# Kernel tuning notes

Hardware: AMD Instinct MI355X
Metric: run time of the kernel (lower is better)

The kernel has to match this reference:

```python
import jax, jax.numpy as jnp
import numpy as np

N_NODES = 50000  # nodes in the (sub)graph


def setup_inputs() -> dict:
    key = jax.random.key(0)
    ks = jax.random.split(key, 8)
    nodes = jax.random.randint(ks[0], (N_NODES,), 0, 100000)
    src = jax.random.randint(ks[1], (800000,), 0, N_NODES)
    dst = jax.random.randint(ks[2], (800000,), 0, N_NODES)
    emb = jax.random.normal(ks[3], (100000, 256), dtype=jnp.float32)
    W = jax.random.normal(ks[4], (256, 128), dtype=jnp.float32) * 0.05
    b = jax.random.normal(ks[5], (128,), dtype=jnp.float32) * 0.05
    mlp_w = jax.random.normal(ks[6], (128, 40), dtype=jnp.float32) * 0.05
    mlp_b = jax.random.normal(ks[7], (40,), dtype=jnp.float32) * 0.05
    return {"nodes": nodes, "src": src, "dst": dst, "emb": emb,
            "W": W, "b": b, "mlp_w": mlp_w, "mlp_b": mlp_b}


def reference(nodes, src, dst, emb, W, b, mlp_w, mlp_b):
    n = N_NODES
    ones = jnp.ones_like(src, dtype=jnp.float32)
    out_deg = jax.ops.segment_sum(ones, src, num_segments=n)  # src out-degree
    in_deg = jax.ops.segment_sum(ones, dst, num_segments=n)   # dst in-degree
    norm_src = jax.lax.rsqrt(jnp.maximum(out_deg, 1.0))       # D_out^{-1/2}
    norm_dst = jax.lax.rsqrt(jnp.maximum(in_deg, 1.0))        # D_in^{-1/2}

    feat = emb[nodes]                                          # [N, in_dim]
    # dgl GraphConv(norm='both'): in_dim > out_dim -> project first, then aggregate
    h = (feat * norm_src[:, None]) @ W                         # [N, out_dim]
    agg = jax.ops.segment_sum(h[src], dst, num_segments=n)     # SpMM: sum over in-edges
    feat_out = agg * norm_dst[:, None] + b                     # [N, out_dim]

    logits = feat_out @ mlp_w + mlp_b                          # [N, num_classes]
    return (feat_out, logits)
```

## Files before the change

kernel.cpp:

```cpp
#include <hip/hip_runtime.h>

#define IN_DIM 256
#define OUT_DIM 128
#define N_CLS 40

#define SLICE 8192
#define NE_CH 20

typedef __attribute__((ext_vector_type(8))) short short8;
typedef __attribute__((ext_vector_type(4))) float floatx4;

static __device__ __forceinline__ unsigned short f2bf(float f) {
    union { float f; unsigned u; } v; v.f = f;
    unsigned r = v.u + 0x7FFF + ((v.u >> 16) & 1);
    return (unsigned short)(r >> 16);
}

__global__ __launch_bounds__(256) void hist_wconv_kernel(
    const int* __restrict__ src, const int* __restrict__ dst,
    int* __restrict__ partial_out, int* __restrict__ partial_in,
    const float* __restrict__ W, unsigned short* __restrict__ Wt,
    int ne, int n, int chunk, int nbh)
{
    __shared__ __align__(16) int lh_out[SLICE];
    __shared__ __align__(16) int lh_in[SLICE];

    const int tid = threadIdx.x;

    if (blockIdx.x >= nbh) {
        int t = (blockIdx.x - nbh) * 256 + tid;
        if (t < IN_DIM * OUT_DIM) {
            int k = t >> 7, c = t & 127;
            Wt[c * IN_DIM + k] = f2bf(W[t]);
        }
        return;
    }

    const int s = blockIdx.x / NE_CH;
    const int e = blockIdx.x % NE_CH;
    const int lo = s * SLICE;
    const int hi = min(lo + SLICE, n);

    for (int i = tid; i < SLICE; i += 256) { lh_out[i] = 0; lh_in[i] = 0; }
    __syncthreads();

    const int start = e * chunk;
    const int end = min(start + chunk, ne);
    const int cnt4 = (end - start) >> 2;
    const int4* s4 = (const int4*)(src + start);
    const int4* d4 = (const int4*)(dst + start);
    for (int k = tid; k < cnt4; k += 256) {
        int4 sv = s4[k];
        int4 dv = d4[k];
        unsigned q;
        q = (unsigned)(sv.x - lo); if (q < SLICE) atomicAdd(&lh_out[q], 1);
        q = (unsigned)(sv.y - lo); if (q < SLICE) atomicAdd(&lh_out[q], 1);
        q = (unsigned)(sv.z - lo); if (q < SLICE) atomicAdd(&lh_out[q], 1);
        q = (unsigned)(sv.w - lo); if (q < SLICE) atomicAdd(&lh_out[q], 1);
        q = (unsigned)(dv.x - lo); if (q < SLICE) atomicAdd(&lh_in[q], 1);
        q = (unsigned)(dv.y - lo); if (q < SLICE) atomicAdd(&lh_in[q], 1);
        q = (unsigned)(dv.z - lo); if (q < SLICE) atomicAdd(&lh_in[q], 1);
        q = (unsigned)(dv.w - lo); if (q < SLICE) atomicAdd(&lh_in[q], 1);
    }
    for (int t = start + (cnt4 << 2) + tid; t < end; t += 256) {
        unsigned q;
        q = (unsigned)(src[t] - lo); if (q < SLICE) atomicAdd(&lh_out[q], 1);
        q = (unsigned)(dst[t] - lo); if (q < SLICE) atomicAdd(&lh_in[q], 1);
    }
    __syncthreads();

    const int cnt = hi - lo;
    const int c4 = cnt >> 2;
    int4* po = (int4*)(partial_out + (size_t)e * n + lo);
    int4* pi = (int4*)(partial_in + (size_t)e * n + lo);
    for (int i = tid; i < c4; i += 256) {
        po[i] = ((const int4*)lh_out)[i];
        pi[i] = ((const int4*)lh_in)[i];
    }
    for (int i = (c4 << 2) + tid; i < cnt; i += 256) {
        partial_out[(size_t)e * n + lo + i] = lh_out[i];
        partial_in[(size_t)e * n + lo + i] = lh_in[i];
    }
}

__global__ __launch_bounds__(256) void reduce_kernel(
    int* __restrict__ partial_out, int* __restrict__ partial_in,
    int* __restrict__ cnt_out, int* __restrict__ cnt_in, int n)
{
    const int g = blockIdx.x * 256 + threadIdx.x;
    const int ng4 = n >> 2;
    if (g < ng4) {
        const size_t base = (size_t)g * 4;
        int4 sum = make_int4(0, 0, 0, 0);
#pragma unroll
        for (int e = 0; e < NE_CH; e++) {
            int4 v = *(const int4*)(partial_out + (size_t)e * n + base);
            sum.x += v.x; sum.y += v.y; sum.z += v.z; sum.w += v.w;
        }
        *(int4*)(cnt_out + base) = sum;

        int4 run = make_int4(0, 0, 0, 0);
#pragma unroll
        for (int e = 0; e < NE_CH; e++) {
            int* p = partial_in + (size_t)e * n + base;
            int4 v = *(const int4*)p;
            *(int4*)p = run;
            run.x += v.x; run.y += v.y; run.z += v.z; run.w += v.w;
        }
        *(int4*)(cnt_in + base) = run;
    }
    const int t = (ng4 << 2) + g;
    if (t < n) {
        int sum = 0;
#pragma unroll
        for (int e = 0; e < NE_CH; e++) sum += partial_out[(size_t)e * n + t];
        cnt_out[t] = sum;
        int run = 0;
#pragma unroll
        for (int e = 0; e < NE_CH; e++) {
            int v = partial_in[(size_t)e * n + t];
            partial_in[(size_t)e * n + t] = run;
            run += v;
        }
        cnt_in[t] = run;
    }
}

__global__ __launch_bounds__(1024) void scan_kernel(
    const int* __restrict__ cnt, int* __restrict__ row_start, int n)
{
    __shared__ int wsum[16];
    __shared__ int carry_s;
    const int tid = threadIdx.x;
    const int lane = tid & 63, wid = tid >> 6;
    if (tid == 0) carry_s = 0;
    __syncthreads();

    for (int chunk = 0; chunk < n; chunk += 8192) {
        int base = chunk + tid * 8;
        int v[8];
        if (base + 8 <= n) {
            int4 a = *(const int4*)&cnt[base];
            int4 b = *(const int4*)&cnt[base + 4];
            v[0]=a.x; v[1]=a.y; v[2]=a.z; v[3]=a.w;
            v[4]=b.x; v[5]=b.y; v[6]=b.z; v[7]=b.w;
        } else {
#pragma unroll
            for (int t = 0; t < 8; t++) v[t] = (base + t < n) ? cnt[base + t] : 0;
        }
        int tsum = 0;
#pragma unroll
        for (int t = 0; t < 8; t++) tsum += v[t];

        int incl = tsum;
#pragma unroll
        for (int off = 1; off < 64; off <<= 1) {
            int q = __shfl_up(incl, (unsigned)off, 64);
            if (lane >= off) incl += q;
        }
        if (lane == 63) wsum[wid] = incl;
        __syncthreads();
        int woff = 0;
        for (int w = 0; w < wid; ++w) woff += wsum[w];
        int carry = carry_s;
        int run = carry + woff + (incl - tsum);
        if (base + 8 <= n) {
            int o[8];
#pragma unroll
            for (int t = 0; t < 8; t++) { o[t] = run; run += v[t]; }
            int4 r0, r1;
            r0.x=o[0]; r0.y=o[1]; r0.z=o[2]; r0.w=o[3];
            r1.x=o[4]; r1.y=o[5]; r1.z=o[6]; r1.w=o[7];
            *(int4*)&row_start[base]     = r0;
            *(int4*)&row_start[base + 4] = r1;
        } else {
#pragma unroll
            for (int t = 0; t < 8; t++) {
                if (base + t < n) row_start[base + t] = run;
                run += v[t];
            }
        }
        __syncthreads();
        if (tid == 1023) carry_s = carry + woff + incl;
        __syncthreads();
    }
    if (tid == 0) row_start[n] = carry_s;
}

__global__ __launch_bounds__(256) void scatter_lds_kernel(
    const int* __restrict__ src, const int* __restrict__ dst,
    const int* __restrict__ row_start, const int* __restrict__ prefix_in,
    int* __restrict__ csr_src, int ne, int n, int chunk)
{
    __shared__ __align__(16) int cur[SLICE];

    const int tid = threadIdx.x;
    const int s = blockIdx.x / NE_CH;
    const int e = blockIdx.x % NE_CH;
    const int lo = s * SLICE;
    const int hi = min(lo + SLICE, n);
    const int cnt = hi - lo;

    const int c4 = cnt >> 2;
    for (int i = tid; i < c4; i += 256) {
        int4 rs = *(const int4*)(row_start + lo + i * 4);
        int4 pf = *(const int4*)(prefix_in + (size_t)e * n + lo + i * 4);
        rs.x += pf.x; rs.y += pf.y; rs.z += pf.z; rs.w += pf.w;
        ((int4*)cur)[i] = rs;
    }
    for (int i = (c4 << 2) + tid; i < cnt; i += 256)
        cur[i] = row_start[lo + i] + prefix_in[(size_t)e * n + lo + i];
    __syncthreads();

    const int start = e * chunk;
    const int end = min(start + chunk, ne);
    const int cnt4e = (end - start) >> 2;
    const int4* s4 = (const int4*)(src + start);
    const int4* d4 = (const int4*)(dst + start);
    for (int k = tid; k < cnt4e; k += 256) {
        int4 sv = s4[k];
        int4 dv = d4[k];
        unsigned q;
        q = (unsigned)(dv.x - lo); if (q < SLICE) csr_src[atomicAdd(&cur[q], 1)] = sv.x;
        q = (unsigned)(dv.y - lo); if (q < SLICE) csr_src[atomicAdd(&cur[q], 1)] = sv.y;
        q = (unsigned)(dv.z - lo); if (q < SLICE) csr_src[atomicAdd(&cur[q], 1)] = sv.z;
        q = (unsigned)(dv.w - lo); if (q < SLICE) csr_src[atomicAdd(&cur[q], 1)] = sv.w;
    }
    for (int t = start + (cnt4e << 2) + tid; t < end; t += 256) {
        unsigned q = (unsigned)(dst[t] - lo);
        if (q < SLICE) csr_src[atomicAdd(&cur[q], 1)] = src[t];
    }
}

__global__ __launch_bounds__(256) void gemm1_mfma_kernel(
    const int* __restrict__ nodes, const float* __restrict__ emb,
    const unsigned short* __restrict__ Wt, const int* __restrict__ cnt_out,
    unsigned short* __restrict__ h, int n)
{
    __shared__ unsigned short A_lds[128 * 40];
    __shared__ unsigned short B_lds[128 * 40];
    __shared__ int   snode[128];
    __shared__ float sscale[128];

    const int tid = threadIdx.x;
    const int m0  = blockIdx.x * 128;

    if (tid < 128) {
        int gr = m0 + tid;
        snode[tid]  = (gr < n) ? nodes[gr] : 0;
        sscale[tid] = (gr < n) ? rsqrtf(fmaxf((float)cnt_out[gr], 1.0f)) : 0.0f;
    }
    __syncthreads();

    const int arow = tid >> 1, aq = tid & 1;
    const float* aptr = emb + (size_t)snode[arow] * IN_DIM + aq * 16;
    const unsigned short* bptr = Wt + arow * IN_DIM + aq * 16;

    float    ar[16];
    unsigned bw[8];

#define LOAD_REGS(KK) do {                                           \
        _Pragma("unroll")                                            \
        for (int q = 0; q < 4; q++) {                                \
            const floatx4 v = *(const floatx4*)(aptr + (KK) * 32 + q * 4); \
            ar[q*4+0]=v[0]; ar[q*4+1]=v[1]; ar[q*4+2]=v[2]; ar[q*4+3]=v[3]; \
        }                                                            \
        const uint4 w0 = *(const uint4*)(bptr + (KK) * 32);          \
        const uint4 w1 = *(const uint4*)(bptr + (KK) * 32 + 8);      \
        bw[0]=w0.x; bw[1]=w0.y; bw[2]=w0.z; bw[3]=w0.w;              \
        bw[4]=w1.x; bw[5]=w1.y; bw[6]=w1.z; bw[7]=w1.w;              \
    } while (0)

#define WRITE_LDS() do {                                             \
        union { unsigned short s[16]; uint4 v[2]; } ua;              \
        _Pragma("unroll")                                            \
        for (int i = 0; i < 16; i++) ua.s[i] = f2bf(ar[i]);          \
        *(uint4*)&A_lds[arow * 40 + aq * 16]     = ua.v[0];          \
        *(uint4*)&A_lds[arow * 40 + aq * 16 + 8] = ua.v[1];          \
        uint4 b0, b1;                                                \
        b0.x=bw[0]; b0.y=bw[1]; b0.z=bw[2]; b0.w=bw[3];              \
        b1.x=bw[4]; b1.y=bw[5]; b1.z=bw[6]; b1.w=bw[7];              \
        *(uint4*)&B_lds[arow * 40 + aq * 16]     = b0;               \
        *(uint4*)&B_lds[arow * 40 + aq * 16 + 8] = b1;               \
    } while (0)

    const int wave = tid >> 6, lane = tid & 63;
    const int wr = (wave & 1) * 64;
    const int wc = (wave >> 1) * 64;
    const int fr = lane & 15;
    const int koff = (lane >> 4) * 8;

    floatx4 acc[4][4];
#pragma unroll
    for (int i = 0; i < 4; i++)
#pragma unroll
        for (int j = 0; j < 4; j++) acc[i][j] = (floatx4){0.f, 0.f, 0.f, 0.f};

    LOAD_REGS(0);
    WRITE_LDS();

    for (int kk = 0; kk < 8; ++kk) {
        if (kk < 7) LOAD_REGS(kk + 1);
        __syncthreads();
        short8 af[4], bf[4];
#pragma unroll
        for (int t = 0; t < 4; t++) {
            af[t] = *(const short8*)&A_lds[(wr + t * 16 + fr) * 40 + koff];
            bf[t] = *(const short8*)&B_lds[(wc + t * 16 + fr) * 40 + koff];
        }
#pragma unroll
        for (int rt = 0; rt < 4; rt++)
#pragma unroll
            for (int ct = 0; ct < 4; ct++)
                acc[rt][ct] = __builtin_amdgcn_mfma_f32_16x16x32_bf16(
                    bf[ct], af[rt], acc[rt][ct], 0, 0, 0);
        __syncthreads();
        if (kk < 7) WRITE_LDS();
    }

#pragma unroll
    for (int rt = 0; rt < 4; rt++) {
        int lrow = wr + rt * 16 + fr;
        int grow = m0 + lrow;
        float sc = sscale[lrow];
        if (grow < n) {
#pragma unroll
            for (int ct = 0; ct < 4; ct++) {
                int col = wc + ct * 16 + (lane >> 4) * 4;
                union { unsigned short s[4]; uint2 v; } o;
                o.s[0] = f2bf(acc[rt][ct][0] * sc);
                o.s[1] = f2bf(acc[rt][ct][1] * sc);
                o.s[2] = f2bf(acc[rt][ct][2] * sc);
                o.s[3] = f2bf(acc[rt][ct][3] * sc);
                *(uint2*)&h[(size_t)grow * OUT_DIM + col] = o.v;
            }
        }
    }
#undef LOAD_REGS
#undef WRITE_LDS
}

__global__ __launch_bounds__(256) void spmm_csr_kernel(
    const int* __restrict__ row_start, const int* __restrict__ csr_src,
    const unsigned short* __restrict__ h, const float* __restrict__ bias,
    float* __restrict__ out_feat, int n)
{
    const int lane = threadIdx.x & 63;
    const int c2 = lane * 2;
    const int row = blockIdx.x * 4 + (threadIdx.x >> 6);
    if (row >= n) return;

    const int rs = row_start[row];
    const int re = row_start[row + 1];
    const int deg = re - rs;

    float aL[4] = {0.f, 0.f, 0.f, 0.f};
    float aH[4] = {0.f, 0.f, 0.f, 0.f};

    for (int base = 0; base < deg; base += 64) {
        const int cnt = min(deg - base, 64);
        int idx = (lane < cnt) ? csr_src[rs + base + lane] : 0;
        int t = 0;
        for (; t + 15 < cnt; t += 16) {
            int s[16];
#pragma unroll
            for (int u = 0; u < 16; u++) s[u] = __shfl(idx, t + u, 64);
            unsigned v[16];
#pragma unroll
            for (int u = 0; u < 16; u++)
                v[u] = *(const unsigned*)&h[(size_t)s[u] * OUT_DIM + c2];
#pragma unroll
            for (int u = 0; u < 16; u++) {
                union { unsigned uu; float f; } x, y;
                x.uu = v[u] << 16;
                y.uu = v[u] & 0xffff0000u;
                aL[u & 3] += x.f;
                aH[u & 3] += y.f;
            }
        }
        for (; t + 3 < cnt; t += 4) {
            int s[4];
#pragma unroll
            for (int u = 0; u < 4; u++) s[u] = __shfl(idx, t + u, 64);
            unsigned v[4];
#pragma unroll
            for (int u = 0; u < 4; u++)
                v[u] = *(const unsigned*)&h[(size_t)s[u] * OUT_DIM + c2];
#pragma unroll
            for (int u = 0; u < 4; u++) {
                union { unsigned uu; float f; } x, y;
                x.uu = v[u] << 16;
                y.uu = v[u] & 0xffff0000u;
                aL[u] += x.f;
                aH[u] += y.f;
            }
        }
        for (; t < cnt; ++t) {
            int s0 = __shfl(idx, t, 64);
            unsigned v0 = *(const unsigned*)&h[(size_t)s0 * OUT_DIM + c2];
            union { unsigned uu; float f; } x, y;
            x.uu = v0 << 16;
            y.uu = v0 & 0xffff0000u;
            aL[0] += x.f;
            aH[0] += y.f;
        }
    }

    const float nd = rsqrtf(fmaxf((float)deg, 1.0f));
    const float f0 = ((aL[0] + aL[1]) + (aL[2] + aL[3])) * nd + bias[c2];
    const float f1 = ((aH[0] + aH[1]) + (aH[2] + aH[3])) * nd + bias[c2 + 1];
    union { float f[2]; unsigned long long u; } o;
    o.f[0] = f0; o.f[1] = f1;
    __builtin_nontemporal_store(o.u,
        (unsigned long long*)&out_feat[(size_t)row * OUT_DIM + c2]);
}

__global__ __launch_bounds__(256) void mlp_mfma_kernel(
    const float* __restrict__ F, const float* __restrict__ mlp_w,
    const float* __restrict__ mlp_b, float* __restrict__ out_logits, int n)
{
    __shared__ unsigned short A_lds[48 * 136];
    __shared__ float s_mlpb[48];

    const int tid = threadIdx.x;
    for (int i = tid; i < 48 * 128; i += 256) {
        int cls = i >> 7, k = i & 127;
        A_lds[cls * 136 + k] =
            (cls < N_CLS) ? f2bf(mlp_w[(size_t)k * N_CLS + cls]) : (unsigned short)0;
    }
    if (tid < 48) s_mlpb[tid] = (tid < N_CLS) ? mlp_b[tid] : 0.f;
    __syncthreads();

    const int wave = tid >> 6, lane = tid & 63;
    const int r = lane & 15, koff = (lane >> 4) * 8;
    const int row = blockIdx.x * 64 + wave * 16 + r;
    const int rowc = (row < n) ? row : (n - 1);
    const float* fp = F + (size_t)rowc * OUT_DIM + koff;

    floatx4 acc[3];
#pragma unroll
    for (int ct = 0; ct < 3; ct++) acc[ct] = (floatx4){0.f, 0.f, 0.f, 0.f};

#pragma unroll
    for (int kk = 0; kk < 4; kk++) {
        floatx4 v0 = *(const floatx4*)(fp + kk * 32);
        floatx4 v1 = *(const floatx4*)(fp + kk * 32 + 4);
        union { unsigned short s[8]; short8 v; } bfr;
#pragma unroll
        for (int i = 0; i < 4; i++) {
            bfr.s[i]     = f2bf(v0[i]);
            bfr.s[4 + i] = f2bf(v1[i]);
        }
#pragma unroll
        for (int ct = 0; ct < 3; ct++) {
            short8 af = *(const short8*)&A_lds[(ct * 16 + r) * 136 + kk * 32 + koff];
            acc[ct] = __builtin_amdgcn_mfma_f32_16x16x32_bf16(af, bfr.v, acc[ct], 0, 0, 0);
        }
    }

    if (row < n) {
#pragma unroll
        for (int ct = 0; ct < 3; ct++)
#pragma unroll
            for (int i = 0; i < 4; i++) {
                int cls = ct * 16 + (lane >> 4) * 4 + i;
                if (cls < N_CLS)
                    __builtin_nontemporal_store(acc[ct][i] + s_mlpb[cls],
                        &out_logits[(size_t)row * N_CLS + cls]);
            }
    }
}

extern "C" void kernel_launch(void* const* d_in, const int* in_sizes, int n_in,
                              void* d_out, int out_size, void* d_ws, size_t ws_size,
                              hipStream_t stream) {
    const int*   nodes = (const int*)d_in[0];
    const int*   src   = (const int*)d_in[1];
    const int*   dst   = (const int*)d_in[2];
    const float* emb   = (const float*)d_in[3];
    const float* W     = (const float*)d_in[4];
    const float* b     = (const float*)d_in[5];
    const float* mlp_w = (const float*)d_in[6];
    const float* mlp_b = (const float*)d_in[7];

    const int n  = in_sizes[0];
    const int ne = in_sizes[1];

    int* cnt_out     = (int*)d_ws;
    int* cnt_in      = cnt_out + n;
    int* row_start   = cnt_in + n;
    int* csr_src     = row_start + n + 8;
    int* partial_out = csr_src + ne;
    int* partial_in  = partial_out + (size_t)NE_CH * n;
    size_t off = ((size_t)(3 * n + 8) + (size_t)ne + 2 * (size_t)NE_CH * n) * sizeof(int);
    off = (off + 15) & ~(size_t)15;
    unsigned short* Wt = (unsigned short*)((char*)d_ws + off);
    off += (size_t)IN_DIM * OUT_DIM * sizeof(unsigned short);
    off = (off + 15) & ~(size_t)15;
    unsigned short* h = (unsigned short*)((char*)d_ws + off);

    float* out_feat   = (float*)d_out;
    float* out_logits = out_feat + (size_t)n * OUT_DIM;

    const int ns = (n + SLICE - 1) / SLICE;
    const int chunk = (((ne + NE_CH - 1) / NE_CH) + 3) & ~3;
    const int nbh = ns * NE_CH;
    const int nbw = (IN_DIM * OUT_DIM + 255) / 256;

    hist_wconv_kernel<<<nbh + nbw, 256, 0, stream>>>(
        src, dst, partial_out, partial_in, W, Wt, ne, n, chunk, nbh);
    reduce_kernel<<<((n >> 2) + 255) / 256, 256, 0, stream>>>(
        partial_out, partial_in, cnt_out, cnt_in, n);
    scan_kernel<<<1, 1024, 0, stream>>>(cnt_in, row_start, n);
    scatter_lds_kernel<<<nbh, 256, 0, stream>>>(
        src, dst, row_start, partial_in, csr_src, ne, n, chunk);
    gemm1_mfma_kernel<<<(n + 127) / 128, 256, 0, stream>>>(nodes, emb, Wt, cnt_out, h, n);
    spmm_csr_kernel<<<(n + 3) / 4, 256, 0, stream>>>(
        row_start, csr_src, h, b, out_feat, n);
    mlp_mfma_kernel<<<(n + 63) / 64, 256, 0, stream>>>(
        out_feat, mlp_w, mlp_b, out_logits, n);
}
```

Before: 152.0 us.

## Split h into two column halves and run SpMM as two half-width passes

The GEMM now writes its bf16 output as two separate [N,64] column-half arrays, and the SpMM runs twice, once per half, each gathering one 2-byte element per lane. The aim is to shrink the gather working set per pass so the randomly accessed rows of h stay in cache better. In exchange, the CSR indices are read twice, there is an extra launch, and each gathered row segment becomes 128 bytes per wave with 16-bit loads. Separately, the histogram slice size and edge chunk count are doubled, which changes the block count and LDS use of the histogram and scatter kernels.

```diff
diff --git a/kernel.cpp b/kernel.cpp
--- a/kernel.cpp
+++ b/kernel.cpp
@@ -4,8 +4,8 @@
 #define OUT_DIM 128
 #define N_CLS 40
 
-#define SLICE 8192
-#define NE_CH 20
+#define SLICE 16384
+#define NE_CH 40
 
 typedef __attribute__((ext_vector_type(8))) short short8;
 typedef __attribute__((ext_vector_type(4))) float floatx4;
@@ -235,7 +235,7 @@
 __global__ __launch_bounds__(256) void gemm1_mfma_kernel(
     const int* __restrict__ nodes, const float* __restrict__ emb,
     const unsigned short* __restrict__ Wt, const int* __restrict__ cnt_out,
-    unsigned short* __restrict__ h, int n)
+    unsigned short* __restrict__ h0, unsigned short* __restrict__ h1, int n)
 {
     __shared__ unsigned short A_lds[128 * 40];
     __shared__ unsigned short B_lds[128 * 40];
@@ -318,6 +318,7 @@
         if (kk < 7) WRITE_LDS();
     }
 
+    unsigned short* hb = wc ? h1 : h0;
 #pragma unroll
     for (int rt = 0; rt < 4; rt++) {
         int lrow = wr + rt * 16 + fr;
@@ -326,13 +327,13 @@
         if (grow < n) {
 #pragma unroll
             for (int ct = 0; ct < 4; ct++) {
-                int col = wc + ct * 16 + (lane >> 4) * 4;
+                int col = ct * 16 + (lane >> 4) * 4;
                 union { unsigned short s[4]; uint2 v; } o;
                 o.s[0] = f2bf(acc[rt][ct][0] * sc);
                 o.s[1] = f2bf(acc[rt][ct][1] * sc);
                 o.s[2] = f2bf(acc[rt][ct][2] * sc);
                 o.s[3] = f2bf(acc[rt][ct][3] * sc);
-                *(uint2*)&h[(size_t)grow * OUT_DIM + col] = o.v;
+                *(uint2*)&hb[(size_t)grow * 64 + col] = o.v;
             }
         }
     }
@@ -340,13 +341,14 @@
 #undef WRITE_LDS
 }
 
-__global__ __launch_bounds__(256) void spmm_csr_kernel(
+__global__ __launch_bounds__(256) void spmm_half_kernel(
     const int* __restrict__ row_start, const int* __restrict__ csr_src,
-    const unsigned short* __restrict__ h, const float* __restrict__ bias,
-    float* __restrict__ out_feat, int n)
+    const unsigned short* __restrict__ hh,
+    const float* __restrict__ bias_half,
+    float* __restrict__ out_col,
+    int n)
 {
     const int lane = threadIdx.x & 63;
-    const int c2 = lane * 2;
     const int row = blockIdx.x * 4 + (threadIdx.x >> 6);
     if (row >= n) return;
 
@@ -354,8 +356,7 @@
     const int re = row_start[row + 1];
     const int deg = re - rs;
 
-    float aL[4] = {0.f, 0.f, 0.f, 0.f};
-    float aH[4] = {0.f, 0.f, 0.f, 0.f};
+    float a[4] = {0.f, 0.f, 0.f, 0.f};
 
     for (int base = 0; base < deg; base += 64) {
         const int cnt = min(deg - base, 64);
@@ -365,54 +366,41 @@
             int s[16];
 #pragma unroll
             for (int u = 0; u < 16; u++) s[u] = __shfl(idx, t + u, 64);
-            unsigned v[16];
-#pragma unroll
-            for (int u = 0; u < 16; u++)
-                v[u] = *(const unsigned*)&h[(size_t)s[u] * OUT_DIM + c2];
+            unsigned short v[16];
+#pragma unroll
+            for (int u = 0; u < 16; u++) v[u] = hh[(size_t)s[u] * 64 + lane];
 #pragma unroll
             for (int u = 0; u < 16; u++) {
-                union { unsigned uu; float f; } x, y;
-                x.uu = v[u] << 16;
-                y.uu = v[u] & 0xffff0000u;
-                aL[u & 3] += x.f;
-                aH[u & 3] += y.f;
+                union { unsigned uu; float f; } x;
+                x.uu = ((unsigned)v[u]) << 16;
+                a[u & 3] += x.f;
             }
         }
         for (; t + 3 < cnt; t += 4) {
             int s[4];
 #pragma unroll
             for (int u = 0; u < 4; u++) s[u] = __shfl(idx, t + u, 64);
-            unsigned v[4];
-#pragma unroll
-            for (int u = 0; u < 4; u++)
-                v[u] = *(const unsigned*)&h[(size_t)s[u] * OUT_DIM + c2];
+            unsigned short v[4];
+#pragma unroll
+            for (int u = 0; u < 4; u++) v[u] = hh[(size_t)s[u] * 64 + lane];
 #pragma unroll
             for (int u = 0; u < 4; u++) {
-                union { unsigned uu; float f; } x, y;
-                x.uu = v[u] << 16;
-                y.uu = v[u] & 0xffff0000u;
-                aL[u] += x.f;
-                aH[u] += y.f;
+                union { unsigned uu; float f; } x;
+                x.uu = ((unsigned)v[u]) << 16;
+                a[u] += x.f;
             }
         }
         for (; t < cnt; ++t) {
             int s0 = __shfl(idx, t, 64);
-            unsigned v0 = *(const unsigned*)&h[(size_t)s0 * OUT_DIM + c2];
-            union { unsigned uu; float f; } x, y;
-            x.uu = v0 << 16;
-            y.uu = v0 & 0xffff0000u;
-            aL[0] += x.f;
-            aH[0] += y.f;
+            union { unsigned uu; float f; } x;
+            x.uu = ((unsigned)hh[(size_t)s0 * 64 + lane]) << 16;
+            a[0] += x.f;
         }
     }
 
     const float nd = rsqrtf(fmaxf((float)deg, 1.0f));
-    const float f0 = ((aL[0] + aL[1]) + (aL[2] + aL[3])) * nd + bias[c2];
-    const float f1 = ((aH[0] + aH[1]) + (aH[2] + aH[3])) * nd + bias[c2 + 1];
-    union { float f[2]; unsigned long long u; } o;
-    o.f[0] = f0; o.f[1] = f1;
-    __builtin_nontemporal_store(o.u,
-        (unsigned long long*)&out_feat[(size_t)row * OUT_DIM + c2]);
+    const float f0 = ((a[0] + a[1]) + (a[2] + a[3])) * nd + bias_half[lane];
+    __builtin_nontemporal_store(f0, &out_col[(size_t)row * OUT_DIM + lane]);
 }
 
 __global__ __launch_bounds__(256) void mlp_mfma_kernel(
@@ -497,7 +485,8 @@
     unsigned short* Wt = (unsigned short*)((char*)d_ws + off);
     off += (size_t)IN_DIM * OUT_DIM * sizeof(unsigned short);
     off = (off + 15) & ~(size_t)15;
-    unsigned short* h = (unsigned short*)((char*)d_ws + off);
+    unsigned short* h0 = (unsigned short*)((char*)d_ws + off);
+    unsigned short* h1 = h0 + (size_t)n * 64;
 
     float* out_feat   = (float*)d_out;
     float* out_logits = out_feat + (size_t)n * OUT_DIM;
@@ -514,9 +503,12 @@
     scan_kernel<<<1, 1024, 0, stream>>>(cnt_in, row_start, n);
     scatter_lds_kernel<<<nbh, 256, 0, stream>>>(
         src, dst, row_start, partial_in, csr_src, ne, n, chunk);
-    gemm1_mfma_kernel<<<(n + 127) / 128, 256, 0, stream>>>(nodes, emb, Wt, cnt_out, h, n);
-    spmm_csr_kernel<<<(n + 3) / 4, 256, 0, stream>>>(
-        row_start, csr_src, h, b, out_feat, n);
+    gemm1_mfma_kernel<<<(n + 127) / 128, 256, 0, stream>>>(
+        nodes, emb, Wt, cnt_out, h0, h1, n);
+    spmm_half_kernel<<<(n + 3) / 4, 256, 0, stream>>>(
+        row_start, csr_src, h0, b, out_feat, n);
+    spmm_half_kernel<<<(n + 3) / 4, 256, 0, stream>>>(
+        row_start, csr_src, h1, b + 64, out_feat + 64, n);
     mlp_mfma_kernel<<<(n + 63) / 64, 256, 0, stream>>>(
         out_feat, mlp_w, mlp_b, out_logits, n);
 }
```

Result: no change. 152.6 us (+0.4%).
